# Performance work log

Measured on AMD Instinct MI355X. Metric: run time of the kernel, lower is better.

## Reference

```python
import jax, jax.numpy as jnp
import numpy as np

B, N, T, F, H, HEADS, E, EDIM, P = 4, 1000, 8, 64, 64, 4, 16000, 16, 5
NEG_SLOPE = 0.2


def _seg_softmax(e, seg, n):
    # segment softmax over destination nodes; every segment is nonempty (self-loops)
    m = jax.ops.segment_max(e, seg, num_segments=n)
    ex = jnp.exp(e - m[seg])
    s = jax.ops.segment_sum(ex, seg, num_segments=n)
    return ex / s[seg]


def _gat(x, ei, W, a_src, a_dst, b):
    # PyG GATConv with concat=False (mean over heads), self-loops already in ei
    n = x.shape[0]
    heads, hh = a_src.shape
    h = (x @ W).reshape(n, heads, hh)                       # [N, heads, H]
    asrc = (h * a_src).sum(-1)                              # [N, heads]
    adst = (h * a_dst).sum(-1)
    src, dst = ei[0], ei[1]
    e = jax.nn.leaky_relu(asrc[src] + adst[dst], NEG_SLOPE)  # [E2, heads]
    alpha = _seg_softmax(e, dst, n)
    out = jax.ops.segment_sum(alpha[:, :, None] * h[src], dst, num_segments=n)
    return out.mean(1) + b                                   # [N, H]


def _gru_cell(x, h, Wih, Whh, bih, bhh):
    gi = x @ Wih.T + bih
    gh = h @ Whh.T + bhh
    i_r, i_z, i_n = jnp.split(gi, 3, axis=-1)
    h_r, h_z, h_n = jnp.split(gh, 3, axis=-1)
    r = jax.nn.sigmoid(i_r + h_r)
    z = jax.nn.sigmoid(i_z + h_z)
    nn_ = jnp.tanh(i_n + r * h_n)
    return (1.0 - z) * nn_ + z * h


def setup_inputs() -> dict:
    key = jax.random.key(0)
    ks = jax.random.split(key, 20)
    rn = lambda k, shp, s: (jax.random.normal(k, shp, jnp.float32) * s)
    inp = {}
    inp['x'] = jax.random.normal(ks[0], (B, N, T, F), jnp.float32)
    inp['edge_index_seq'] = jax.random.randint(ks[1], (B, T, 2, E), 0, N)
    inp['edge_feat_seq'] = jax.random.normal(ks[2], (B, T, E, EDIM), jnp.float32)
    inp['W1'] = rn(ks[3], (F, HEADS * H), 1 / np.sqrt(F))
    inp['att_src1'] = rn(ks[4], (HEADS, H), 1 / np.sqrt(H))
    inp['att_dst1'] = rn(ks[5], (HEADS, H), 1 / np.sqrt(H))
    inp['b1'] = jnp.zeros((H,), jnp.float32)
    inp['W2'] = rn(ks[6], (H, HEADS * H), 1 / np.sqrt(H))
    inp['att_src2'] = rn(ks[7], (HEADS, H), 1 / np.sqrt(H))
    inp['att_dst2'] = rn(ks[8], (HEADS, H), 1 / np.sqrt(H))
    inp['b2'] = jnp.zeros((H,), jnp.float32)
    inp['edge_W'] = rn(ks[9], (EDIM, H), 1 / np.sqrt(EDIM))
    inp['edge_b'] = jnp.zeros((H,), jnp.float32)
    inp['Wih0'] = rn(ks[10], (3 * H, H), 1 / np.sqrt(H))
    inp['Whh0'] = rn(ks[11], (3 * H, H), 1 / np.sqrt(H))
    inp['bih0'] = jnp.zeros((3 * H,), jnp.float32)
    inp['bhh0'] = jnp.zeros((3 * H,), jnp.float32)
    inp['Wih1'] = rn(ks[12], (3 * H, H), 1 / np.sqrt(H))
    inp['Whh1'] = rn(ks[13], (3 * H, H), 1 / np.sqrt(H))
    inp['bih1'] = jnp.zeros((3 * H,), jnp.float32)
    inp['bhh1'] = jnp.zeros((3 * H,), jnp.float32)
    inp['pW1'] = rn(ks[14], (H, H), 1 / np.sqrt(H))
    inp['pb1'] = jnp.zeros((H,), jnp.float32)
    inp['pW2'] = rn(ks[15], (H, 2 * P), 1 / np.sqrt(H))
    inp['pb2'] = jnp.zeros((2 * P,), jnp.float32)
    return inp


def reference(x, edge_index_seq, edge_feat_seq, W1, att_src1, att_dst1, b1,
              W2, att_src2, att_dst2, b2, edge_W, edge_b,
              Wih0, Whh0, bih0, bhh0, Wih1, Whh1, bih1, bhh1,
              pW1, pb1, pW2, pb2):
    Bs, Ns, Ts, Fs = x.shape
    G = Bs * Ts
    # [B,N,T,F] -> [B*T, N, F] (graph per (b,t))
    xg = x.transpose(0, 2, 1, 3).reshape(G, Ns, Fs)
    ei = edge_index_seq.reshape(G, 2, -1)
    # add self-loops (PyG GATConv default)
    sl = jnp.broadcast_to(jnp.arange(Ns), (G, 2, Ns))
    ei = jnp.concatenate([ei, sl], axis=-1)

    def per_graph(xt, e):
        h = jax.nn.relu(_gat(xt, e, W1, att_src1, att_dst1, b1))
        return _gat(h, e, W2, att_src2, att_dst2, b2)

    h = jax.vmap(per_graph)(xg, ei)                         # [G, N, H]
    Hd = h.shape[-1]
    # note: original computes edge_embedding(edge_feat) but never uses it (dead code)
    h = h.reshape(Bs, Ts, Ns, Hd).transpose(0, 2, 1, 3).reshape(Bs * Ns, Ts, Hd)
    xs = h.transpose(1, 0, 2)                               # [T, B*N, H]
    h0 = jnp.zeros((Bs * Ns, Hd), x.dtype)

    def step(carry, xt):
        h1, h2 = carry
        h1n = _gru_cell(xt, h1, Wih0, Whh0, bih0, bhh0)
        h2n = _gru_cell(h1n, h2, Wih1, Whh1, bih1, bhh1)
        return (h1n, h2n), None

    (_, hT), _ = jax.lax.scan(step, (h0, h0), xs)           # hT: [B*N, H]
    mid = jax.nn.relu(hT @ pW1 + pb1)
    pred = mid @ pW2 + pb2                                  # [B*N, 2P]
    return pred.reshape(Bs, Ns, P, 2)
```

## Files before the change

kernel.cpp:

```cpp
#include <hip/hip_runtime.h>
#include <math.h>

#define BB 4
#define NN 1000
#define TT 8
#define FF 64
#define HH 64
#define NHEADS 4
#define EE 16000
#define E2 17000
#define GG (BB*TT)
#define GN (GG*NN)
#define NROWS (BB*NN)

__device__ __forceinline__ float sigmoidf_(float x) {
    return 1.f / (1.f + __expf(-x));
}
__device__ __forceinline__ float tanhf_(float x) {
    x = fminf(fmaxf(x, -15.f), 15.f);
    float e = __expf(2.f * x);
    return (e - 1.f) / (e + 1.f);
}
__device__ __forceinline__ float leaky_(float x) {
    return (x > 0.f) ? x : 0.2f * x;
}

__global__ void count_edges(const int* __restrict__ ei, int* __restrict__ counts) {
    int g = blockIdx.y;
    int e = blockIdx.x * 256 + threadIdx.x;
    if (e >= E2) return;
    int dst;
    if (e < EE) dst = ei[(size_t)g * 2 * EE + EE + e];
    else        dst = e - EE;
    atomicAdd(&counts[g * NN + dst], 1);
}

__global__ __launch_bounds__(256) void scan_offsets_pg(const int* __restrict__ counts,
                                                       int* __restrict__ offs) {
    __shared__ int tot[256];
    int g = blockIdx.x;
    int tid = threadIdx.x;
    int base = tid * 4;
    int c0 = 0, c1 = 0, c2 = 0, c3 = 0;
    if (base < NN) {
        int4 v = *(const int4*)(counts + (size_t)g * NN + base);
        c0 = v.x; c1 = v.y; c2 = v.z; c3 = v.w;
    }
    int s = c0 + c1 + c2 + c3;
    tot[tid] = s;
    __syncthreads();
    for (int off = 1; off < 256; off <<= 1) {
        int y = (tid >= off) ? tot[tid - off] : 0;
        __syncthreads();
        tot[tid] += y;
        __syncthreads();
    }
    int run = g * E2 + tot[tid] - s;
    if (base < NN) {
        int4 o;
        o.x = run; run += c0;
        o.y = run; run += c1;
        o.z = run; run += c2;
        o.w = run;
        *(int4*)(offs + (size_t)g * NN + base) = o;
    }
    if (g == 0 && tid == 0) offs[GN] = GG * E2;
}

__global__ void scatter_edges(const int* __restrict__ ei, const int* __restrict__ offs,
                              int* __restrict__ cursor, int* __restrict__ csr) {
    int g = blockIdx.y;
    int e = blockIdx.x * 256 + threadIdx.x;
    if (e >= E2) return;
    int src, dst;
    if (e < EE) {
        src = ei[(size_t)g * 2 * EE + e];
        dst = ei[(size_t)g * 2 * EE + EE + e];
    } else {
        src = dst = e - EE;
    }
    int i = g * NN + dst;
    int pos = offs[i] + atomicAdd(&cursor[i], 1);
    csr[pos] = src;
}

#define PIN64_(arr)                                        \
    _Pragma("unroll")                                      \
    for (int _pi = 0; _pi < 64; ++_pi)                     \
        asm volatile("" : "+v"((arr)[_pi]));

template <int MODE>
__global__ __launch_bounds__(256) void gat_linear(
    const float* __restrict__ in, const float* __restrict__ W,
    const float* __restrict__ att_s, const float* __restrict__ att_d,
    float* __restrict__ hlin, float* __restrict__ asrc, float* __restrict__ adst) {
    const int ROWS = 10;
    const int CH = NN / ROWS;
    int g = blockIdx.x / CH;
    int n0 = (blockIdx.x % CH) * ROWS;
    int tid = threadIdx.x;
    float wcol[FF];
#pragma unroll
    for (int f = 0; f < FF; ++f) wcol[f] = W[f * 256 + tid];
    int head = tid >> 6, lane = tid & 63;
    float as = att_s[head * HH + lane];
    float ad = att_d[head * HH + lane];
    int b = g / TT, t = g % TT;
    for (int r = 0; r < ROWS; ++r) {
        int n = n0 + r;
        const float* xrow;
        if (MODE == 0) xrow = in + (((size_t)(b * NN + n) * TT + t) * FF);
        else           xrow = in + ((size_t)(g * NN + n) * FF);
        float acc = 0.f;
#pragma unroll
        for (int f = 0; f < FF; ++f) acc = fmaf(xrow[f], wcol[f], acc);
        hlin[((size_t)(g * NN + n) << 8) + (lane << 2) + head] = acc;
        float s1 = acc * as, s2 = acc * ad;
#pragma unroll
        for (int off = 32; off; off >>= 1) {
            s1 += __shfl_xor(s1, off, 64);
            s2 += __shfl_xor(s2, off, 64);
        }
        if (lane == 0) {
            asrc[(size_t)(g * NN + n) * NHEADS + head] = s1;
            adst[(size_t)(g * NN + n) * NHEADS + head] = s2;
        }
    }
}

__global__ __launch_bounds__(256) void gat_edge(
    const float* __restrict__ hlin, const float* __restrict__ asrc,
    const float* __restrict__ adst, const int* __restrict__ offs,
    const int* __restrict__ csr, const float* __restrict__ bias,
    float* __restrict__ out, int do_relu) {
    __shared__ float pbuf[4][64][4];
    __shared__ int   sbuf[4][64];
    __shared__ int   degs[4];
    int tid = threadIdx.x;
    int lane = tid & 63, w = tid >> 6;
    int B = blockIdx.x;
    int x = B & 7, j = B >> 3;
    int graph = x + 8 * (j / 250);
    int node = graph * NN + ((j % 250) << 2) + w;
    int beg = offs[node], end = offs[node + 1];
    int deg = end - beg;
    if (lane == 0) degs[w] = deg;
    __syncthreads();
    int maxdeg = max(max(degs[0], degs[1]), max(degs[2], degs[3]));
    int nchunk = (maxdeg + 63) >> 6;

    float4 ad = *(const float4*)(adst + (size_t)node * 4);
    const float* asrc_g = asrc + (size_t)graph * NN * 4;
    const float* hg = hlin + ((size_t)graph * NN << 8);

    float4 acc = make_float4(0.f, 0.f, 0.f, 0.f);
    float4 ssum = make_float4(0.f, 0.f, 0.f, 0.f);
    for (int c = 0; c < nchunk; ++c) {
        int e0 = beg + (c << 6);
        int myedge = e0 + lane;
        float4 p = make_float4(0.f, 0.f, 0.f, 0.f);
        int src = 0;
        if (myedge < end) {
            src = csr[myedge];
            float4 a = *(const float4*)(asrc_g + (size_t)src * 4);
            p.x = __expf(leaky_(a.x + ad.x));
            p.y = __expf(leaky_(a.y + ad.y));
            p.z = __expf(leaky_(a.z + ad.z));
            p.w = __expf(leaky_(a.w + ad.w));
        }
        float4 t = p;
#pragma unroll
        for (int off = 1; off < 64; off <<= 1) {
            t.x += __shfl_xor(t.x, off, 64);
            t.y += __shfl_xor(t.y, off, 64);
            t.z += __shfl_xor(t.z, off, 64);
            t.w += __shfl_xor(t.w, off, 64);
        }
        ssum.x += t.x; ssum.y += t.y; ssum.z += t.z; ssum.w += t.w;
        *(float4*)&pbuf[w][lane][0] = p;
        sbuf[w][lane] = src;
        __syncthreads();
        int cnt = end - e0;
        if (cnt > 64) cnt = 64;
        int cnt8 = (cnt + 7) & ~7;
        for (int e = 0; e < cnt8; e += 8) {
            float4 p0 = *(const float4*)&pbuf[w][e + 0][0];
            float4 p1 = *(const float4*)&pbuf[w][e + 1][0];
            float4 p2 = *(const float4*)&pbuf[w][e + 2][0];
            float4 p3 = *(const float4*)&pbuf[w][e + 3][0];
            float4 p4 = *(const float4*)&pbuf[w][e + 4][0];
            float4 p5 = *(const float4*)&pbuf[w][e + 5][0];
            float4 p6 = *(const float4*)&pbuf[w][e + 6][0];
            float4 p7 = *(const float4*)&pbuf[w][e + 7][0];
            int s0 = sbuf[w][e + 0], s1 = sbuf[w][e + 1];
            int s2 = sbuf[w][e + 2], s3 = sbuf[w][e + 3];
            int s4 = sbuf[w][e + 4], s5 = sbuf[w][e + 5];
            int s6 = sbuf[w][e + 6], s7 = sbuf[w][e + 7];
            int lo = lane << 2;
            float4 h0 = *(const float4*)(hg + (((size_t)s0) << 8) + lo);
            float4 h1 = *(const float4*)(hg + (((size_t)s1) << 8) + lo);
            float4 h2 = *(const float4*)(hg + (((size_t)s2) << 8) + lo);
            float4 h3 = *(const float4*)(hg + (((size_t)s3) << 8) + lo);
            float4 h4 = *(const float4*)(hg + (((size_t)s4) << 8) + lo);
            float4 h5 = *(const float4*)(hg + (((size_t)s5) << 8) + lo);
            float4 h6 = *(const float4*)(hg + (((size_t)s6) << 8) + lo);
            float4 h7 = *(const float4*)(hg + (((size_t)s7) << 8) + lo);
            acc.x = fmaf(p0.x, h0.x, acc.x); acc.y = fmaf(p0.y, h0.y, acc.y);
            acc.z = fmaf(p0.z, h0.z, acc.z); acc.w = fmaf(p0.w, h0.w, acc.w);
            acc.x = fmaf(p1.x, h1.x, acc.x); acc.y = fmaf(p1.y, h1.y, acc.y);
            acc.z = fmaf(p1.z, h1.z, acc.z); acc.w = fmaf(p1.w, h1.w, acc.w);
            acc.x = fmaf(p2.x, h2.x, acc.x); acc.y = fmaf(p2.y, h2.y, acc.y);
            acc.z = fmaf(p2.z, h2.z, acc.z); acc.w = fmaf(p2.w, h2.w, acc.w);
            acc.x = fmaf(p3.x, h3.x, acc.x); acc.y = fmaf(p3.y, h3.y, acc.y);
            acc.z = fmaf(p3.z, h3.z, acc.z); acc.w = fmaf(p3.w, h3.w, acc.w);
            acc.x = fmaf(p4.x, h4.x, acc.x); acc.y = fmaf(p4.y, h4.y, acc.y);
            acc.z = fmaf(p4.z, h4.z, acc.z); acc.w = fmaf(p4.w, h4.w, acc.w);
            acc.x = fmaf(p5.x, h5.x, acc.x); acc.y = fmaf(p5.y, h5.y, acc.y);
            acc.z = fmaf(p5.z, h5.z, acc.z); acc.w = fmaf(p5.w, h5.w, acc.w);
            acc.x = fmaf(p6.x, h6.x, acc.x); acc.y = fmaf(p6.y, h6.y, acc.y);
            acc.z = fmaf(p6.z, h6.z, acc.z); acc.w = fmaf(p6.w, h6.w, acc.w);
            acc.x = fmaf(p7.x, h7.x, acc.x); acc.y = fmaf(p7.y, h7.y, acc.y);
            acc.z = fmaf(p7.z, h7.z, acc.z); acc.w = fmaf(p7.w, h7.w, acc.w);
        }
        __syncthreads();
    }
    float o = 0.25f * (acc.x / ssum.x + acc.y / ssum.y + acc.z / ssum.z + acc.w / ssum.w)
            + bias[lane];
    if (do_relu) o = fmaxf(o, 0.f);
    out[((size_t)node << 6) + lane] = o;
}

template <int MODE>
__global__ __launch_bounds__(192, 4) void gru_gi(
    const float* __restrict__ in, const float* __restrict__ Wih,
    const float* __restrict__ bih, float* __restrict__ giseq) {
    const int ROWS = 10;
    int j = threadIdx.x;
    float wrow[64];
#pragma unroll
    for (int f4 = 0; f4 < 16; ++f4) {
        float4 w = *(const float4*)(Wih + (size_t)j * 64 + f4 * 4);
        wrow[4 * f4 + 0] = w.x; wrow[4 * f4 + 1] = w.y;
        wrow[4 * f4 + 2] = w.z; wrow[4 * f4 + 3] = w.w;
    }
    PIN64_(wrow)
    float bj = bih[j];
    int q0 = blockIdx.x * ROWS;
    int t = q0 / NROWS;
    int r0 = q0 - t * NROWS;
    for (int rr = 0; rr < ROWS; rr += 2) {
        const float *xa, *xb;
        if (MODE == 0) {
            int ra = r0 + rr, rb = ra + 1;
            int ba = ra / NN, na = ra - ba * NN;
            int bb2 = rb / NN, nb = rb - bb2 * NN;
            xa = in + (((size_t)(ba * TT + t) * NN + na) << 6);
            xb = in + (((size_t)(bb2 * TT + t) * NN + nb) << 6);
        } else {
            xa = in + ((size_t)(q0 + rr) << 6);
            xb = xa + 64;
        }
        float acca = bj, accb = bj;
#pragma unroll
        for (int f4 = 0; f4 < 16; ++f4) {
            float4 a4 = *(const float4*)(xa + f4 * 4);
            float4 b4 = *(const float4*)(xb + f4 * 4);
            acca = fmaf(a4.x, wrow[4 * f4 + 0], acca);
            acca = fmaf(a4.y, wrow[4 * f4 + 1], acca);
            acca = fmaf(a4.z, wrow[4 * f4 + 2], acca);
            acca = fmaf(a4.w, wrow[4 * f4 + 3], acca);
            accb = fmaf(b4.x, wrow[4 * f4 + 0], accb);
            accb = fmaf(b4.y, wrow[4 * f4 + 1], accb);
            accb = fmaf(b4.z, wrow[4 * f4 + 2], accb);
            accb = fmaf(b4.w, wrow[4 * f4 + 3], accb);
        }
        giseq[(size_t)(q0 + rr) * 192 + j] = acca;
        giseq[(size_t)(q0 + rr + 1) * 192 + j] = accb;
    }
}

template <int LAYER>
__global__ __launch_bounds__(128) void gru_rec(
    const float* __restrict__ giseq, const float* __restrict__ Whh,
    const float* __restrict__ bhh, float* __restrict__ outseq) {
    __shared__ float hs[4][64];
    int tid = threadIdx.x;
    int ch = tid & 63, w = tid >> 6;
    float wr[64], wz[64], wn[64];
#pragma unroll
    for (int k4 = 0; k4 < 16; ++k4) {
        float4 a = *(const float4*)(Whh + (size_t)ch * 64 + k4 * 4);
        float4 b = *(const float4*)(Whh + (size_t)(64 + ch) * 64 + k4 * 4);
        float4 c = *(const float4*)(Whh + (size_t)(128 + ch) * 64 + k4 * 4);
        wr[4*k4+0] = a.x; wr[4*k4+1] = a.y; wr[4*k4+2] = a.z; wr[4*k4+3] = a.w;
        wz[4*k4+0] = b.x; wz[4*k4+1] = b.y; wz[4*k4+2] = b.z; wz[4*k4+3] = b.w;
        wn[4*k4+0] = c.x; wn[4*k4+1] = c.y; wn[4*k4+2] = c.z; wn[4*k4+3] = c.w;
    }
    float br = bhh[ch], bz = bhh[64 + ch], bn = bhh[128 + ch];
    int row0 = blockIdx.x * 4 + w * 2;
    float hprev[2];
#pragma unroll
    for (int r = 0; r < 2; ++r) { hs[w * 2 + r][ch] = 0.f; hprev[r] = 0.f; }

    for (int t = 0; t < TT; ++t) {
#pragma unroll
        for (int r = 0; r < 2; ++r) {
            int row = row0 + r;
            const float* gp = giseq + ((size_t)(t * NROWS + row)) * 192;
            float gir = gp[ch], giz = gp[64 + ch], gin = gp[128 + ch];
            float ar = br, az = bz, an = bn;
#pragma unroll
            for (int k4 = 0; k4 < 16; ++k4) {
                float4 h4 = *(const float4*)&hs[w * 2 + r][k4 * 4];
                ar = fmaf(h4.x, wr[4*k4+0], ar); ar = fmaf(h4.y, wr[4*k4+1], ar);
                ar = fmaf(h4.z, wr[4*k4+2], ar); ar = fmaf(h4.w, wr[4*k4+3], ar);
                az = fmaf(h4.x, wz[4*k4+0], az); az = fmaf(h4.y, wz[4*k4+1], az);
                az = fmaf(h4.z, wz[4*k4+2], az); az = fmaf(h4.w, wz[4*k4+3], az);
                an = fmaf(h4.x, wn[4*k4+0], an); an = fmaf(h4.y, wn[4*k4+1], an);
                an = fmaf(h4.z, wn[4*k4+2], an); an = fmaf(h4.w, wn[4*k4+3], an);
            }
            float rg = sigmoidf_(gir + ar);
            float zg = sigmoidf_(giz + az);
            float ng = tanhf_(gin + rg * an);
            float hnew = (1.f - zg) * ng + zg * hprev[r];
            hprev[r] = hnew;
            hs[w * 2 + r][ch] = hnew;
            if (LAYER == 0)
                outseq[(((size_t)(t * NROWS + row)) << 6) + ch] = hnew;
        }
    }
    if (LAYER == 1) {
#pragma unroll
        for (int r = 0; r < 2; ++r)
            outseq[(((size_t)(row0 + r)) << 6) + ch] = hprev[r];
    }
}

__global__ __launch_bounds__(64) void mlp_head(
    const float* __restrict__ hT, const float* __restrict__ pW1,
    const float* __restrict__ pb1, const float* __restrict__ pW2,
    const float* __restrict__ pb2, float* __restrict__ out) {
    int r = blockIdx.x, lane = threadIdx.x;
    __shared__ float hrow[64];
    __shared__ float mid[64];
    hrow[lane] = hT[((size_t)r << 6) + lane];
    __syncthreads();
    float acc = pb1[lane];
#pragma unroll
    for (int k = 0; k < 64; ++k) acc = fmaf(hrow[k], pW1[k * 64 + lane], acc);
    mid[lane] = fmaxf(acc, 0.f);
    __syncthreads();
    if (lane < 10) {
        float o = pb2[lane];
#pragma unroll
        for (int k = 0; k < 64; ++k) o = fmaf(mid[k], pW2[k * 10 + lane], o);
        out[(size_t)r * 10 + lane] = o;
    }
}

extern "C" void kernel_launch(void* const* d_in, const int* in_sizes, int n_in,
                              void* d_out, int out_size, void* d_ws, size_t ws_size,
                              hipStream_t stream) {
    (void)in_sizes; (void)n_in; (void)out_size; (void)ws_size;
    const float* x    = (const float*)d_in[0];
    const int*   ei   = (const int*)d_in[1];
    const float* W1   = (const float*)d_in[3];
    const float* as1  = (const float*)d_in[4];
    const float* ad1  = (const float*)d_in[5];
    const float* b1   = (const float*)d_in[6];
    const float* W2   = (const float*)d_in[7];
    const float* as2  = (const float*)d_in[8];
    const float* ad2  = (const float*)d_in[9];
    const float* b2   = (const float*)d_in[10];
    const float* Wih0 = (const float*)d_in[13];
    const float* Whh0 = (const float*)d_in[14];
    const float* bih0 = (const float*)d_in[15];
    const float* bhh0 = (const float*)d_in[16];
    const float* Wih1 = (const float*)d_in[17];
    const float* Whh1 = (const float*)d_in[18];
    const float* bih1 = (const float*)d_in[19];
    const float* bhh1 = (const float*)d_in[20];
    const float* pW1  = (const float*)d_in[21];
    const float* pb1  = (const float*)d_in[22];
    const float* pW2  = (const float*)d_in[23];
    const float* pb2  = (const float*)d_in[24];
    float* out = (float*)d_out;

    char* ws = (char*)d_ws;
    float* hlin  = (float*)(ws + 0);
    float* giseq = hlin;
    float* asrc  = (float*)(ws + 32768000);
    float* hT    = asrc;
    float* adst  = (float*)(ws + 33280000);
    float* gat1  = (float*)(ws + 33792000);
    float* h1seq = gat1;
    float* gat2  = (float*)(ws + 41984000);
    int* counts  = (int*)(ws + 50176000);
    int* cursor  = (int*)(ws + 50304000);
    int* offs    = (int*)(ws + 50432000);
    int* csr     = (int*)(ws + 50560256);

    hipMemsetAsync(counts, 0, 2 * GN * sizeof(int), stream);

    dim3 egrid((E2 + 255) / 256, GG);
    count_edges<<<egrid, 256, 0, stream>>>(ei, counts);
    scan_offsets_pg<<<GG, 256, 0, stream>>>(counts, offs);
    scatter_edges<<<egrid, 256, 0, stream>>>(ei, offs, cursor, csr);

    gat_linear<0><<<GG * 100, 256, 0, stream>>>(x, W1, as1, ad1, hlin, asrc, adst);
    gat_edge<<<GN / 4, 256, 0, stream>>>(hlin, asrc, adst, offs, csr, b1, gat1, 1);
    gat_linear<1><<<GG * 100, 256, 0, stream>>>(gat1, W2, as2, ad2, hlin, asrc, adst);
    gat_edge<<<GN / 4, 256, 0, stream>>>(hlin, asrc, adst, offs, csr, b2, gat2, 0);

    gru_gi<0><<<3200, 192, 0, stream>>>(gat2, Wih0, bih0, giseq);
    gru_rec<0><<<1000, 128, 0, stream>>>(giseq, Whh0, bhh0, h1seq);
    gru_gi<1><<<3200, 192, 0, stream>>>(h1seq, Wih1, bih1, giseq);
    gru_rec<1><<<1000, 128, 0, stream>>>(giseq, Whh1, bhh1, hT);

    mlp_head<<<NROWS, 64, 0, stream>>>(hT, pW1, pb1, pW2, pb2, out);
}
```

Baseline: 416.6 us.

## Compute GAT linear projections with split-bf16 MFMA instead of scalar FMA

Replaces the scalar FP32 GAT linear kernel with a bf16 MFMA GEMM that uses a hi/lo bf16 split of both operands to approximate FP32 accuracy. New prep kernels pack the inputs and weights into an MFMA fragment layout, and the attention dot products are reduced from the accumulators with shuffles. The aim is to move the projection work onto the matrix cores. In exchange it adds two extra launches per layer, a packed-buffer round trip through memory, and eight MFMAs per tile for the precision emulation.

```diff
diff --git a/kernel.cpp b/kernel.cpp
--- a/kernel.cpp
+++ b/kernel.cpp
@@ -13,6 +13,9 @@
 #define GN (GG*NN)
 #define NROWS (BB*NN)
 
+typedef __attribute__((ext_vector_type(8))) short bf16x8;
+typedef __attribute__((ext_vector_type(4))) float f32x4;
+
 __device__ __forceinline__ float sigmoidf_(float x) {
     return 1.f / (1.f + __expf(-x));
 }
@@ -23,6 +26,10 @@
 }
 __device__ __forceinline__ float leaky_(float x) {
     return (x > 0.f) ? x : 0.2f * x;
+}
+__device__ __forceinline__ ushort bf16_rne(float v) {
+    uint b = __float_as_uint(v);
+    return (ushort)((b + 0x7FFF + ((b >> 16) & 1)) >> 16);
 }
 
 __global__ void count_edges(const int* __restrict__ ei, int* __restrict__ counts) {
@@ -89,41 +96,167 @@
     for (int _pi = 0; _pi < 64; ++_pi)                     \
         asm volatile("" : "+v"((arr)[_pi]));
 
+
 template <int MODE>
-__global__ __launch_bounds__(256) void gat_linear(
-    const float* __restrict__ in, const float* __restrict__ W,
+__global__ __launch_bounds__(256) void xprep(
+    const float* __restrict__ in, ushort* __restrict__ ap) {
+    int g = blockIdx.x / 63, mt = blockIdx.x % 63;
+    int tid = threadIdx.x;
+    int xq = tid >> 7, kb = (tid >> 6) & 1, row = (tid >> 2) & 15, koct = tid & 3;
+    int n = mt * 16 + row;
+    int f0 = kb * 32 + koct * 8;
+    float v[8];
+    if (n < NN) {
+        const float* xr;
+        if (MODE == 0) {
+            int b = g / TT, t = g % TT;
+            xr = in + (((size_t)(b * NN + n) * TT + t) * FF);
+        } else {
+            xr = in + ((size_t)(g * NN + n) * FF);
+        }
+        float4 a = *(const float4*)(xr + f0);
+        float4 c = *(const float4*)(xr + f0 + 4);
+        v[0] = a.x; v[1] = a.y; v[2] = a.z; v[3] = a.w;
+        v[4] = c.x; v[5] = c.y; v[6] = c.z; v[7] = c.w;
+    } else {
+#pragma unroll
+        for (int j = 0; j < 8; ++j) v[j] = 0.f;
+    }
+    ushort o[8];
+#pragma unroll
+    for (int j = 0; j < 8; ++j) {
+        ushort h = bf16_rne(v[j]);
+        if (xq == 0) o[j] = h;
+        else {
+            float hf = __uint_as_float(((uint)h) << 16);
+            o[j] = bf16_rne(v[j] - hf);
+        }
+    }
+    size_t off = (size_t)(g * 63 + mt) * 2048
+               + ((size_t)((xq * 2 + kb) * 16 + row) * 4 + koct) * 8;
+    uint4 ow;
+    ow.x = (uint)o[0] | ((uint)o[1] << 16);
+    ow.y = (uint)o[2] | ((uint)o[3] << 16);
+    ow.z = (uint)o[4] | ((uint)o[5] << 16);
+    ow.w = (uint)o[6] | ((uint)o[7] << 16);
+    *(uint4*)(ap + off) = ow;
+}
+
+__global__ __launch_bounds__(64) void wprep(
+    const float* __restrict__ W1, const float* __restrict__ W2,
+    ushort* __restrict__ B1, ushort* __restrict__ B2) {
+    int blk = blockIdx.x;
+    const float* W = (blk >> 6) ? W2 : W1;
+    ushort* Bp = (blk >> 6) ? B2 : B1;
+    int r = blk & 63;
+    int wq = r >> 5, kb = (r >> 4) & 1, nt = r & 15;
+    int tid = threadIdx.x;
+    int col = tid >> 2, koct = tid & 3;
+    int c = nt * 16 + col;
+    ushort o[8];
+#pragma unroll
+    for (int j = 0; j < 8; ++j) {
+        int k = kb * 32 + koct * 8 + j;
+        float v = W[k * 256 + c];
+        ushort h = bf16_rne(v);
+        if (wq == 0) o[j] = h;
+        else {
+            float hf = __uint_as_float(((uint)h) << 16);
+            o[j] = bf16_rne(v - hf);
+        }
+    }
+    size_t off = (((size_t)((wq * 2 + kb) * 16 + nt) * 16 + col) * 4 + koct) * 8;
+    uint4 ow;
+    ow.x = (uint)o[0] | ((uint)o[1] << 16);
+    ow.y = (uint)o[2] | ((uint)o[3] << 16);
+    ow.z = (uint)o[4] | ((uint)o[5] << 16);
+    ow.w = (uint)o[6] | ((uint)o[7] << 16);
+    *(uint4*)(Bp + off) = ow;
+}
+
+__global__ __launch_bounds__(256) void gat_mfma(
+    const ushort* __restrict__ ap, const ushort* __restrict__ bp,
     const float* __restrict__ att_s, const float* __restrict__ att_d,
     float* __restrict__ hlin, float* __restrict__ asrc, float* __restrict__ adst) {
-    const int ROWS = 10;
-    const int CH = NN / ROWS;
-    int g = blockIdx.x / CH;
-    int n0 = (blockIdx.x % CH) * ROWS;
+    int g = blockIdx.x >> 4, band = blockIdx.x & 15;
     int tid = threadIdx.x;
-    float wcol[FF];
-#pragma unroll
-    for (int f = 0; f < FF; ++f) wcol[f] = W[f * 256 + tid];
-    int head = tid >> 6, lane = tid & 63;
-    float as = att_s[head * HH + lane];
-    float ad = att_d[head * HH + lane];
-    int b = g / TT, t = g % TT;
-    for (int r = 0; r < ROWS; ++r) {
-        int n = n0 + r;
-        const float* xrow;
-        if (MODE == 0) xrow = in + (((size_t)(b * NN + n) * TT + t) * FF);
-        else           xrow = in + ((size_t)(g * NN + n) * FF);
-        float acc = 0.f;
-#pragma unroll
-        for (int f = 0; f < FF; ++f) acc = fmaf(xrow[f], wcol[f], acc);
-        hlin[((size_t)(g * NN + n) << 8) + (lane << 2) + head] = acc;
-        float s1 = acc * as, s2 = acc * ad;
-#pragma unroll
-        for (int off = 32; off; off >>= 1) {
-            s1 += __shfl_xor(s1, off, 64);
-            s2 += __shfl_xor(s2, off, 64);
-        }
-        if (lane == 0) {
-            asrc[(size_t)(g * NN + n) * NHEADS + head] = s1;
-            adst[(size_t)(g * NN + n) * NHEADS + head] = s2;
+    int w = tid >> 6, lane = tid & 63;
+    int mt = band * 4 + w;
+    if (mt >= 63) return;
+    int lo = lane & 15, hi = lane >> 4;
+
+    const ushort* abase = ap + (size_t)(g * 63 + mt) * 2048;
+    size_t foff = ((size_t)(lo * 4 + hi)) * 8;
+    bf16x8 Ah0 = *(const bf16x8*)(abase + 0 * 512 + foff);
+    bf16x8 Ah1 = *(const bf16x8*)(abase + 1 * 512 + foff);
+    bf16x8 Al0 = *(const bf16x8*)(abase + 2 * 512 + foff);
+    bf16x8 Al1 = *(const bf16x8*)(abase + 3 * 512 + foff);
+
+    f32x4 acc[16];
+#pragma unroll
+    for (int i = 0; i < 16; ++i) acc[i] = (f32x4){0.f, 0.f, 0.f, 0.f};
+
+#pragma unroll
+    for (int nt = 0; nt < 16; ++nt) {
+        const ushort* bb = bp + (size_t)nt * 512 + foff;
+        bf16x8 Bh0 = *(const bf16x8*)(bb + 0 * 8192);
+        bf16x8 Bh1 = *(const bf16x8*)(bb + 1 * 8192);
+        bf16x8 Bl0 = *(const bf16x8*)(bb + 2 * 8192);
+        bf16x8 Bl1 = *(const bf16x8*)(bb + 3 * 8192);
+        acc[nt] = __builtin_amdgcn_mfma_f32_16x16x32_bf16(Ah0, Bh0, acc[nt], 0, 0, 0);
+        acc[nt] = __builtin_amdgcn_mfma_f32_16x16x32_bf16(Ah1, Bh1, acc[nt], 0, 0, 0);
+        acc[nt] = __builtin_amdgcn_mfma_f32_16x16x32_bf16(Ah0, Bl0, acc[nt], 0, 0, 0);
+        acc[nt] = __builtin_amdgcn_mfma_f32_16x16x32_bf16(Ah1, Bl1, acc[nt], 0, 0, 0);
+        acc[nt] = __builtin_amdgcn_mfma_f32_16x16x32_bf16(Al0, Bh0, acc[nt], 0, 0, 0);
+        acc[nt] = __builtin_amdgcn_mfma_f32_16x16x32_bf16(Al1, Bh1, acc[nt], 0, 0, 0);
+        acc[nt] = __builtin_amdgcn_mfma_f32_16x16x32_bf16(Al0, Bl0, acc[nt], 0, 0, 0);
+        acc[nt] = __builtin_amdgcn_mfma_f32_16x16x32_bf16(Al1, Bl1, acc[nt], 0, 0, 0);
+    }
+
+    float s1[4][4], s2[4][4];
+#pragma unroll
+    for (int r = 0; r < 4; ++r)
+#pragma unroll
+        for (int h = 0; h < 4; ++h) { s1[r][h] = 0.f; s2[r][h] = 0.f; }
+
+#pragma unroll
+    for (int nt = 0; nt < 16; ++nt) {
+        int c = nt * 16 + lo;
+        int head = nt >> 2;
+        int slot = ((c & 63) << 2) + head;
+        float as = att_s[c];
+        float ad = att_d[c];
+#pragma unroll
+        for (int reg = 0; reg < 4; ++reg) {
+            int n = mt * 16 + hi * 4 + reg;
+            float v = acc[nt][reg];
+            if (n < NN)
+                hlin[((size_t)(g * NN + n) << 8) + slot] = v;
+            s1[reg][head] += v * as;
+            s2[reg][head] += v * ad;
+        }
+    }
+#pragma unroll
+    for (int off = 1; off < 16; off <<= 1) {
+#pragma unroll
+        for (int reg = 0; reg < 4; ++reg)
+#pragma unroll
+            for (int h = 0; h < 4; ++h) {
+                s1[reg][h] += __shfl_xor(s1[reg][h], off, 64);
+                s2[reg][h] += __shfl_xor(s2[reg][h], off, 64);
+            }
+    }
+    if (lo == 0) {
+#pragma unroll
+        for (int reg = 0; reg < 4; ++reg) {
+            int n = mt * 16 + hi * 4 + reg;
+            if (n < NN) {
+#pragma unroll
+                for (int h = 0; h < 4; ++h) {
+                    asrc[(size_t)(g * NN + n) * NHEADS + h] = s1[reg][h];
+                    adst[(size_t)(g * NN + n) * NHEADS + h] = s2[reg][h];
+                }
+            }
         }
     }
 }
@@ -395,10 +528,13 @@
     float* gat1  = (float*)(ws + 33792000);
     float* h1seq = gat1;
     float* gat2  = (float*)(ws + 41984000);
+    ushort* Apack = (ushort*)(ws + 41984000);
     int* counts  = (int*)(ws + 50176000);
     int* cursor  = (int*)(ws + 50304000);
     int* offs    = (int*)(ws + 50432000);
     int* csr     = (int*)(ws + 50560256);
+    ushort* Bp1  = (ushort*)(ws + 52736256);
+    ushort* Bp2  = (ushort*)(ws + 52801792);
 
     hipMemsetAsync(counts, 0, 2 * GN * sizeof(int), stream);
 
@@ -407,9 +543,13 @@
     scan_offsets_pg<<<GG, 256, 0, stream>>>(counts, offs);
     scatter_edges<<<egrid, 256, 0, stream>>>(ei, offs, cursor, csr);
 
-    gat_linear<0><<<GG * 100, 256, 0, stream>>>(x, W1, as1, ad1, hlin, asrc, adst);
+    wprep<<<128, 64, 0, stream>>>(W1, W2, Bp1, Bp2);
+
+    xprep<0><<<GG * 63, 256, 0, stream>>>(x, Apack);
+    gat_mfma<<<GG * 16, 256, 0, stream>>>(Apack, Bp1, as1, ad1, hlin, asrc, adst);
     gat_edge<<<GN / 4, 256, 0, stream>>>(hlin, asrc, adst, offs, csr, b1, gat1, 1);
-    gat_linear<1><<<GG * 100, 256, 0, stream>>>(gat1, W2, as2, ad2, hlin, asrc, adst);
+    xprep<1><<<GG * 63, 256, 0, stream>>>(gat1, Apack);
+    gat_mfma<<<GG * 16, 256, 0, stream>>>(Apack, Bp2, as2, ad2, hlin, asrc, adst);
     gat_edge<<<GN / 4, 256, 0, stream>>>(hlin, asrc, adst, offs, csr, b2, gat2, 0);
 
     gru_gi<0><<<3200, 192, 0, stream>>>(gat2, Wih0, bih0, giseq);
```

New measurement: 423.9 us. About the same (+1.8%).
